# Performance work log

Measured on AMD Instinct MI355X. Metric: run time of the kernel, lower is better.

Reference implementation:

```python
import jax, jax.numpy as jnp
import numpy as np

B, S, E = 4, 4096, 1024
H = 16
D = E // H            # per-head dim (k_dim == v_dim == 64)
N_SAMPLE = 1024       # tokens kept per (batch, head)


def setup_inputs() -> dict:
    key = jax.random.key(0)
    ks = jax.random.split(key, 7)
    lim = float(np.sqrt(6.0 / (E + E)))  # xavier_uniform for square weight
    x = jax.random.normal(ks[0], (B, S, E), dtype=jnp.float32)
    Wq = jax.random.uniform(ks[1], (E, E), jnp.float32, -lim, lim)
    Wk = jax.random.uniform(ks[2], (E, E), jnp.float32, -lim, lim)
    Wv = jax.random.uniform(ks[3], (E, E), jnp.float32, -lim, lim)
    bq = jnp.zeros((E,), jnp.float32)
    bk = jnp.zeros((E,), jnp.float32)
    bv = jnp.zeros((E,), jnp.float32)
    return {"x": x, "Wq": Wq, "bq": bq, "Wk": Wk, "bk": bk, "Wv": Wv, "bv": bv}


def reference(x, Wq, bq, Wk, bk, Wv, bv):
    Bs, Sl, Ed = x.shape
    # projections -> [B, H, S, D]
    q = (x @ Wq.T + bq).reshape(Bs, Sl, H, D).transpose(0, 2, 1, 3)
    k = (x @ Wk.T + bk).reshape(Bs, Sl, H, D).transpose(0, 2, 1, 3)
    v = (x @ Wv.T + bv).reshape(Bs, Sl, H, D).transpose(0, 2, 1, 3)

    # cosFormer feature map: relu + cos/sin positional reweighting
    pos = jnp.arange(Sl, dtype=x.dtype)
    theta = (jnp.pi / 2.0) * pos / Sl            # [S]
    cos_w = jnp.cos(theta)[None, None, :, None]  # [1,1,S,1]
    sin_w = jnp.sin(theta)[None, None, :, None]
    qn = jax.nn.relu(q)
    kn = jax.nn.relu(k)
    q_cos, q_sin = qn * cos_w, qn * sin_w
    k_cos, k_sin = kn * cos_w, kn * sin_w

    # token sampler: top-N_SAMPLE tokens by (q*k).sum(-1) per (b,h)
    scores = jnp.sum(q * k, axis=-1)             # [B,H,S]
    _, idx = jax.lax.top_k(scores, N_SAMPLE)     # [B,H,n]

    # global K^T V reductions: [B,H,D,D]
    kv_cos = jnp.einsum("bhsd,bhse->bhde", k_cos, v)
    kv_sin = jnp.einsum("bhsd,bhse->bhde", k_sin, v)

    # gather sampled queries: [B,H,n,D]
    qs_cos = jnp.take_along_axis(q_cos, idx[..., None], axis=2)
    qs_sin = jnp.take_along_axis(q_sin, idx[..., None], axis=2)

    sampled = (jnp.einsum("bhnd,bhde->bhne", qs_cos, kv_cos)
               + jnp.einsum("bhnd,bhde->bhne", qs_sin, kv_sin))  # [B,H,n,D]

    # scatter-add back into zeros at sampled positions
    bi = jnp.arange(Bs)[:, None, None]
    hi = jnp.arange(H)[None, :, None]
    values = jnp.zeros((Bs, H, Sl, D), sampled.dtype).at[bi, hi, idx].add(sampled)

    out = values.transpose(0, 2, 1, 3).reshape(Bs, Sl, H * D)
    return out  # o_proj is Identity (v_dim*num_heads == embed_dim); dropout=0
```

## Files before the change

kernel.cpp:

```cpp
#include <hip/hip_runtime.h>
#include <hip/hip_bf16.h>

#define B_ 4
#define S_ 4096
#define E_ 1024
#define H_ 16
#define D_ 64
#define NS_ 1024
#define M_ (B_*S_)
#define K_ E_
#define DELTA 0.12f
#define BANDCAP 96

typedef __attribute__((ext_vector_type(8))) short bf16x8;
typedef __attribute__((ext_vector_type(4))) float floatx4;

#define THSTEP 0.00038349519697141023f

__device__ inline float bf16_to_f(unsigned short u) {
    return __uint_as_float(((unsigned)u) << 16);
}
__device__ inline unsigned short f_to_bf16(float f) {
    unsigned u = __float_as_uint(f);
    unsigned r = (u + 0x7FFFu + ((u >> 16) & 1u)) >> 16;
    return (unsigned short)r;
}

__device__ inline void gl_lds16(const void* g, void* l) {
    __builtin_amdgcn_global_load_lds(
        (const __attribute__((address_space(1))) void*)g,
        (__attribute__((address_space(3))) void*)l, 16, 0, 0);
}

__global__ __launch_bounds__(256) void split_x_kernel(
    const float* __restrict__ x, ushort* __restrict__ xh)
{
    int i = blockIdx.x * 256 + threadIdx.x;
    float4 v = ((const float4*)x)[i];
    ushort4 hh;
    hh.x = f_to_bf16(v.x); hh.y = f_to_bf16(v.y);
    hh.z = f_to_bf16(v.z); hh.w = f_to_bf16(v.w);
    ((ushort4*)xh)[i] = hh;
}

__global__ __launch_bounds__(256) void split_w_kernel(
    const float* __restrict__ Wq, const float* __restrict__ Wk,
    const float* __restrict__ Wv,
    ushort* __restrict__ Wqh, ushort* __restrict__ Wql,
    ushort* __restrict__ Wkh, ushort* __restrict__ Wkl,
    ushort* __restrict__ Wvh)
{
    int i = blockIdx.x * 256 + threadIdx.x;
    float4 q = ((const float4*)Wq)[i];
    float4 k = ((const float4*)Wk)[i];
    float4 v = ((const float4*)Wv)[i];
    ushort4 h, l;
    h.x=f_to_bf16(q.x); l.x=f_to_bf16(q.x-bf16_to_f(h.x));
    h.y=f_to_bf16(q.y); l.y=f_to_bf16(q.y-bf16_to_f(h.y));
    h.z=f_to_bf16(q.z); l.z=f_to_bf16(q.z-bf16_to_f(h.z));
    h.w=f_to_bf16(q.w); l.w=f_to_bf16(q.w-bf16_to_f(h.w));
    ((ushort4*)Wqh)[i]=h; ((ushort4*)Wql)[i]=l;
    h.x=f_to_bf16(k.x); l.x=f_to_bf16(k.x-bf16_to_f(h.x));
    h.y=f_to_bf16(k.y); l.y=f_to_bf16(k.y-bf16_to_f(h.y));
    h.z=f_to_bf16(k.z); l.z=f_to_bf16(k.z-bf16_to_f(h.z));
    h.w=f_to_bf16(k.w); l.w=f_to_bf16(k.w-bf16_to_f(h.w));
    ((ushort4*)Wkh)[i]=h; ((ushort4*)Wkl)[i]=l;
    h.x=f_to_bf16(v.x); h.y=f_to_bf16(v.y);
    h.z=f_to_bf16(v.z); h.w=f_to_bf16(v.w);
    ((ushort4*)Wvh)[i]=h;
}

__global__ __launch_bounds__(256) void qkv_gemm(
    const ushort* __restrict__ xh,
    const ushort* __restrict__ Wqh, const ushort* __restrict__ Wql,
    const ushort* __restrict__ Wkh, const ushort* __restrict__ Wkl,
    const ushort* __restrict__ Wvh,
    const float* __restrict__ bq, const float* __restrict__ bk,
    const float* __restrict__ bv,
    float* __restrict__ q32, float* __restrict__ k32, ushort* __restrict__ v16)
{
    __shared__ __align__(16) ushort As[128 * 64];
    __shared__ __align__(16) ushort Bsh[128 * 64];
    __shared__ __align__(16) ushort Bsl[128 * 64];

    const int w = blockIdx.z;
    const ushort* Bhp = (w == 0) ? Wqh : (w == 1) ? Wkh : Wvh;
    const ushort* Blp = (w == 0) ? Wql : Wkl;
    const float* bias = (w == 0) ? bq : (w == 1) ? bk : bv;
    const bool lo = (w < 2);

    const int m0 = blockIdx.x * 128;
    const int n0 = blockIdx.y * 128;
    const int t = threadIdx.x;
    const int wave = t >> 6, lane = t & 63;
    const int wm = (wave >> 1) * 64, wn = (wave & 1) * 64;
    const int m16 = lane & 15, quad = lane >> 4;

    floatx4 acc[4][4];
#pragma unroll
    for (int i = 0; i < 4; i++)
#pragma unroll
        for (int j = 0; j < 4; j++) acc[i][j] = (floatx4){0.f, 0.f, 0.f, 0.f};

    int aoff[4], boff[4], lbase[4];
#pragma unroll
    for (int i = 0; i < 4; i++) {
        int slot = i * 256 + t;
        int r = slot >> 3, c = slot & 7, g = c ^ (r & 7);
        aoff[i] = (m0 + r) * K_ + g * 8;
        boff[i] = (n0 + r) * K_ + g * 8;
        lbase[i] = (i * 256 + wave * 64) * 8;
    }

    for (int ks = 0; ks < 16; ++ks) {
        const int kcol = ks * 64;
#pragma unroll
        for (int i = 0; i < 4; i++) {
            gl_lds16(xh + aoff[i] + kcol, &As[lbase[i]]);
            gl_lds16(Bhp + boff[i] + kcol, &Bsh[lbase[i]]);
        }
        if (lo) {
#pragma unroll
            for (int i = 0; i < 4; i++)
                gl_lds16(Blp + boff[i] + kcol, &Bsl[lbase[i]]);
        }
        __syncthreads();

#pragma unroll
        for (int kk = 0; kk < 2; ++kk) {
            bf16x8 af[4], bfr[4];
            const int g = kk * 4 + quad;
#pragma unroll
            for (int mt = 0; mt < 4; ++mt) {
                int r = wm + mt * 16 + m16;
                af[mt] = *(const bf16x8*)&As[(r * 8 + (g ^ (r & 7))) * 8];
            }
#pragma unroll
            for (int nt = 0; nt < 4; ++nt) {
                int r2 = wn + nt * 16 + m16;
                bfr[nt] = *(const bf16x8*)&Bsh[(r2 * 8 + (g ^ (r2 & 7))) * 8];
            }
#pragma unroll
            for (int mt = 0; mt < 4; ++mt)
#pragma unroll
                for (int nt = 0; nt < 4; ++nt)
                    acc[mt][nt] = __builtin_amdgcn_mfma_f32_16x16x32_bf16(
                        af[mt], bfr[nt], acc[mt][nt], 0, 0, 0);
            if (lo) {
#pragma unroll
                for (int nt = 0; nt < 4; ++nt) {
                    int r2 = wn + nt * 16 + m16;
                    bfr[nt] = *(const bf16x8*)&Bsl[(r2 * 8 + (g ^ (r2 & 7))) * 8];
                }
#pragma unroll
                for (int mt = 0; mt < 4; ++mt)
#pragma unroll
                    for (int nt = 0; nt < 4; ++nt)
                        acc[mt][nt] = __builtin_amdgcn_mfma_f32_16x16x32_bf16(
                            af[mt], bfr[nt], acc[mt][nt], 0, 0, 0);
            }
        }
        __syncthreads();
    }

    float biasv[4];
#pragma unroll
    for (int nt = 0; nt < 4; nt++)
        biasv[nt] = bias[n0 + wn + nt * 16 + m16];

    if (w < 2) {
        float* dst = (w == 0) ? q32 : k32;
#pragma unroll
        for (int mt = 0; mt < 4; ++mt)
#pragma unroll
            for (int nt = 0; nt < 4; ++nt) {
                int colg = n0 + wn + nt * 16 + m16;
#pragma unroll
                for (int reg = 0; reg < 4; ++reg) {
                    int rowg = m0 + wm + mt * 16 + quad * 4 + reg;
                    dst[(size_t)rowg * E_ + colg] = acc[mt][nt][reg] + biasv[nt];
                }
            }
    } else {
#pragma unroll
        for (int mt = 0; mt < 4; ++mt)
#pragma unroll
            for (int nt = 0; nt < 4; ++nt) {
                int colg = n0 + wn + nt * 16 + m16;
#pragma unroll
                for (int reg = 0; reg < 4; ++reg) {
                    int rowg = m0 + wm + mt * 16 + quad * 4 + reg;
                    v16[(size_t)rowg * E_ + colg] = f_to_bf16(acc[mt][nt][reg] + biasv[nt]);
                }
            }
    }
}

__global__ __launch_bounds__(256) void scores_kernel(
    const float* __restrict__ q32, const float* __restrict__ k32,
    float* __restrict__ scores)
{
    int wid = blockIdx.x * 4 + (threadIdx.x >> 6);
    int lane = threadIdx.x & 63;
    int s = wid & (S_ - 1);
    int bh = wid >> 12;
    int b = bh >> 4, h = bh & 15;
    size_t addr = (size_t)(b * S_ + s) * E_ + h * 64 + lane;
    float p = q32[addr] * k32[addr];
#pragma unroll
    for (int m = 32; m; m >>= 1) p += __shfl_xor(p, m, 64);
    if (lane == 0) scores[wid] = p;
}

__global__ __launch_bounds__(256) void band_select_kernel(
    const float* __restrict__ scores, int* __restrict__ selidx,
    int* __restrict__ band, int* __restrict__ meta)
{
    __shared__ unsigned keys[4096];
    __shared__ unsigned hist[256];
    __shared__ unsigned suf[256];
    __shared__ unsigned bcast[2];
    __shared__ int cnt_in, cnt_band;

    int bh = blockIdx.x;
    int t = threadIdx.x;
    const float* sc = scores + (size_t)bh * S_;

    for (int i = t; i < 4096; i += 256) {
        unsigned u = __float_as_uint(sc[i]);
        u = (u & 0x80000000u) ? ~u : (u | 0x80000000u);
        keys[i] = u;
    }
    if (t == 0) { cnt_in = 0; cnt_band = 0; }
    __syncthreads();

    unsigned prefix = 0, want = NS_;
    for (int shift = 24; shift >= 0; shift -= 8) {
        hist[t] = 0;
        __syncthreads();
        unsigned pmask = (shift == 24) ? 0u : (0xFFFFFFFFu << (shift + 8));
        for (int i = t; i < 4096; i += 256) {
            unsigned ky = keys[i];
            if ((ky & pmask) == prefix) atomicAdd(&hist[(ky >> shift) & 255u], 1u);
        }
        __syncthreads();
        suf[t] = hist[t];
        __syncthreads();
        for (int off = 1; off < 256; off <<= 1) {
            unsigned add = (t + off < 256) ? suf[t + off] : 0u;
            __syncthreads();
            suf[t] += add;
            __syncthreads();
        }
        unsigned Sb = suf[t];
        unsigned Snx = (t < 255) ? suf[t + 1] : 0u;
        if (Sb >= want && Snx < want) {
            bcast[0] = (unsigned)t;
            bcast[1] = want - Snx;
        }
        __syncthreads();
        prefix = prefix | (bcast[0] << shift);
        want = bcast[1];
        __syncthreads();
    }
    unsigned fb = (prefix & 0x80000000u) ? (prefix ^ 0x80000000u) : ~prefix;
    float Ta = __uint_as_float(fb);
    float Thi = Ta + DELTA, Tlo = Ta - DELTA;

    int* sel = selidx + (size_t)bh * NS_;
    int* bnd = band + (size_t)bh * BANDCAP;
    for (int i = t; i < 4096; i += 256) {
        float v = sc[i];
        if (v > Thi) {
            int p = atomicAdd(&cnt_in, 1);
            sel[p] = i;
        } else if (v >= Tlo) {
            int p = atomicAdd(&cnt_band, 1);
            if (p < BANDCAP) bnd[p] = i;
        }
    }
    __syncthreads();
    if (t == 0) {
        meta[bh * 2 + 0] = cnt_in;
        meta[bh * 2 + 1] = (cnt_band < BANDCAP) ? cnt_band : BANDCAP;
    }
}

__global__ __launch_bounds__(512) void band_exact_kernel(
    const float* __restrict__ x,
    const float* __restrict__ Wq, const float* __restrict__ Wk,
    const int* __restrict__ band, const int* __restrict__ meta,
    double* __restrict__ bscore)
{
    int j = blockIdx.x, bh = blockIdx.y;
    int NB = meta[bh * 2 + 1];
    if (j >= NB) return;
    int b = bh >> 4, h = bh & 15;
    int s = band[(size_t)bh * BANDCAP + j];
    int t = threadIdx.x;
    int wave = t >> 6, lane = t & 63;

    __shared__ float xs[1024];
    __shared__ double qkd[128];

    if (t < 256)
        *(float4*)&xs[t * 4] = *(const float4*)(x + (size_t)(b * S_ + s) * K_ + t * 4);
    __syncthreads();

    const float* Wbase = (wave < 4) ? Wq : Wk;
    int role = wave >> 2;
    int dbase = (wave & 3) * 16;
    const float4* xs4 = (const float4*)xs;

    for (int rr = 0; rr < 16; ++rr) {
        int d = dbase + rr;
        const float4* wrow4 = (const float4*)(Wbase + (size_t)(h * 64 + d) * K_);
        double a = 0.0;
#pragma unroll
        for (int p = 0; p < 4; ++p) {
            float4 wv = wrow4[lane + 64 * p];
            float4 xv = xs4[lane + 64 * p];
            a += (double)xv.x * wv.x + (double)xv.y * wv.y
               + (double)xv.z * wv.z + (double)xv.w * wv.w;
        }
#pragma unroll
        for (int m = 32; m; m >>= 1) a += __shfl_xor(a, m, 64);
        if (lane == 0) qkd[role * 64 + d] = a;
    }
    __syncthreads();

    if (t < 64) {
        double p = qkd[t] * qkd[64 + t];
#pragma unroll
        for (int m = 32; m; m >>= 1) p += __shfl_xor(p, m, 64);
        if (t == 0) bscore[(size_t)bh * BANDCAP + j] = p;
    }
}

__global__ __launch_bounds__(128) void band_rank_kernel(
    const double* __restrict__ bscore, const int* __restrict__ band,
    const int* __restrict__ meta, int* __restrict__ selidx)
{
    __shared__ double sc[BANDCAP];
    __shared__ int bi[BANDCAP];
    int bh = blockIdx.x, t = threadIdx.x;
    int cnt_in = meta[bh * 2 + 0], NB = meta[bh * 2 + 1];
    int need = NS_ - cnt_in;
    if (t < NB) {
        sc[t] = bscore[(size_t)bh * BANDCAP + t];
        bi[t] = band[(size_t)bh * BANDCAP + t];
    }
    __syncthreads();
    if (t < NB) {
        double mine = sc[t]; int myi = bi[t]; int r = 0;
        for (int j2 = 0; j2 < NB; ++j2)
            r += (sc[j2] > mine) || (sc[j2] == mine && bi[j2] < myi);
        if (r < need) selidx[(size_t)bh * NS_ + cnt_in + r] = myi;
    }
}

__global__ __launch_bounds__(256) void kv_partial_kernel(
    const float* __restrict__ k32, const ushort* __restrict__ v16,
    float* __restrict__ kvp)
{
    __shared__ float kls[16 * 64];
    __shared__ float vls[16 * 64];
    int ch = blockIdx.x;
    int bh = blockIdx.y;
    int b = bh >> 4, h = bh & 15;
    int t = threadIdx.x;
    int d0 = (t >> 4) * 4, e0 = (t & 15) * 4;
    int lr = t >> 4, lc = (t & 15) * 4;

    float accC[4][4] = {}, accS[4][4] = {};
    const float* kbase = k32 + (size_t)b * S_ * E_ + h * 64;
    const ushort* vbase = v16 + (size_t)b * S_ * E_ + h * 64;
    int s0 = ch * 256;

    for (int g = 0; g < 16; ++g) {
        int srow = s0 + g * 16 + lr;
        float4 kf = *(const float4*)(kbase + (size_t)srow * E_ + lc);
        ushort4 vu = *(const ushort4*)(vbase + (size_t)srow * E_ + lc);
        __syncthreads();
        *(float4*)&kls[lr * 64 + lc] = kf;
        float4 vf = { bf16_to_f(vu.x), bf16_to_f(vu.y),
                      bf16_to_f(vu.z), bf16_to_f(vu.w) };
        *(float4*)&vls[lr * 64 + lc] = vf;
        __syncthreads();
#pragma unroll 4
        for (int si = 0; si < 16; ++si) {
            int s = s0 + g * 16 + si;
            float th = (float)s * THSTEP;
            float cw = __cosf(th), sw = __sinf(th);
            float4 kf2 = *(const float4*)&kls[si * 64 + d0];
            float4 vf2 = *(const float4*)&vls[si * 64 + e0];
            float kr[4] = { fmaxf(kf2.x, 0.f), fmaxf(kf2.y, 0.f),
                            fmaxf(kf2.z, 0.f), fmaxf(kf2.w, 0.f) };
            float vv[4] = { vf2.x, vf2.y, vf2.z, vf2.w };
            float kc[4], ksn[4];
#pragma unroll
            for (int i = 0; i < 4; i++) { kc[i] = kr[i] * cw; ksn[i] = kr[i] * sw; }
#pragma unroll
            for (int i = 0; i < 4; i++)
#pragma unroll
                for (int jj = 0; jj < 4; jj++) {
                    accC[i][jj] += kc[i] * vv[jj];
                    accS[i][jj] += ksn[i] * vv[jj];
                }
        }
    }
    float* pc = kvp + ((size_t)(bh * 16 + ch) * 2) * 4096;
    float* ps = pc + 4096;
#pragma unroll
    for (int i = 0; i < 4; i++)
#pragma unroll
        for (int jj = 0; jj < 4; jj++) {
            pc[(d0 + i) * 64 + (e0 + jj)] = accC[i][jj];
            ps[(d0 + i) * 64 + (e0 + jj)] = accS[i][jj];
        }
}

__global__ __launch_bounds__(256) void kv_reduce_kernel(
    const float* __restrict__ kvp, float* __restrict__ kv)
{
    int i = blockIdx.x * 256 + threadIdx.x;
    if (i >= 64 * 2 * 4096) return;
    int bh = i >> 13;
    int rem = i & 8191;
    const float* p = kvp + (size_t)bh * 16 * 8192 + rem;
    float a = 0.f;
#pragma unroll
    for (int c = 0; c < 16; c++) a += p[c * 8192];
    kv[i] = a;
}

__global__ __launch_bounds__(256) void sampled_kernel(
    const float* __restrict__ q32, const int* __restrict__ selidx,
    const float* __restrict__ kv, float* __restrict__ out)
{
    __shared__ float kvc[4096];
    __shared__ float kvs[4096];
    __shared__ float qs[256 * 65];
    __shared__ int sidx[256];
    int bh = blockIdx.y;
    int b = bh >> 4, h = bh & 15;
    int t = threadIdx.x;
    int wave = t >> 6, lane = t & 63;

    const float* kvsrc = kv + (size_t)bh * 8192;
    for (int i = t; i < 4096; i += 256) {
        kvc[i] = kvsrc[i];
        kvs[i] = kvsrc[4096 + i];
    }
    sidx[t] = selidx[(size_t)bh * NS_ + blockIdx.x * 256 + t];
    __syncthreads();

    for (int i = 0; i < 64; ++i) {
        int row = wave * 64 + i;
        int sr = sidx[row];
        qs[row * 65 + lane] = q32[(size_t)(b * S_ + sr) * E_ + h * 64 + lane];
    }
    __syncthreads();

    int s = sidx[t];
    float th = (float)s * THSTEP;
    float cw = __cosf(th), sw = __sinf(th);

    float acc[64];
#pragma unroll
    for (int e = 0; e < 64; e++) acc[e] = 0.f;

    for (int d = 0; d < 64; ++d) {
        float qd = fmaxf(qs[t * 65 + d], 0.f);
        float a = qd * cw, bb = qd * sw;
        const float4* pc4 = (const float4*)&kvc[d * 64];
        const float4* ps4 = (const float4*)&kvs[d * 64];
#pragma unroll
        for (int e4 = 0; e4 < 16; e4++) {
            float4 c4 = pc4[e4], s4 = ps4[e4];
            acc[e4 * 4 + 0] += a * c4.x + bb * s4.x;
            acc[e4 * 4 + 1] += a * c4.y + bb * s4.y;
            acc[e4 * 4 + 2] += a * c4.z + bb * s4.z;
            acc[e4 * 4 + 3] += a * c4.w + bb * s4.w;
        }
    }
    __syncthreads();
#pragma unroll
    for (int e = 0; e < 64; e++) qs[t * 65 + e] = acc[e];
    __syncthreads();

    for (int i = 0; i < 64; ++i) {
        int row = wave * 64 + i;
        int sr = sidx[row];
        out[(size_t)(b * S_ + sr) * E_ + h * 64 + lane] = qs[row * 65 + lane];
    }
}

__global__ void zero_kernel(uint4* __restrict__ p, int n16)
{
    int stride = gridDim.x * blockDim.x;
    for (int i = blockIdx.x * blockDim.x + threadIdx.x; i < n16; i += stride)
        p[i] = make_uint4(0u, 0u, 0u, 0u);
}

extern "C" void kernel_launch(void* const* d_in, const int* in_sizes, int n_in,
                              void* d_out, int out_size, void* d_ws, size_t ws_size,
                              hipStream_t stream)
{
    const float* x  = (const float*)d_in[0];
    const float* Wq = (const float*)d_in[1];
    const float* bq = (const float*)d_in[2];
    const float* Wk = (const float*)d_in[3];
    const float* bk = (const float*)d_in[4];
    const float* Wv = (const float*)d_in[5];
    const float* bv = (const float*)d_in[6];

    char* ws = (char*)d_ws;
    ushort* xh     = (ushort*)(ws);
    float*  kvp    = (float*)(ws);
    float*  q32    = (float*)(ws + 33554432);
    float*  k32    = (float*)(ws + 100663296);
    ushort* v16    = (ushort*)(ws + 167772160);
    ushort* Wqh    = (ushort*)(ws + 201326592);
    ushort* Wql    = (ushort*)(ws + 203423744);
    ushort* Wkh    = (ushort*)(ws + 205520896);
    ushort* Wkl    = (ushort*)(ws + 207618048);
    ushort* Wvh    = (ushort*)(ws + 209715200);
    float*  scores = (float*)(ws + 211812352);
    int*    selidx = (int*)(ws + 212860928);
    int*    band   = (int*)(ws + 213123072);
    double* bscore = (double*)(ws + 213147648);
    int*    meta   = (int*)(ws + 213196800);
    float*  kv     = (float*)(ws + 213197312);
    float*  out    = (float*)d_out;

    hipLaunchKernelGGL(zero_kernel, dim3(2048), dim3(256), 0, stream,
                       (uint4*)out, (int)((size_t)M_ * E_ * 4 / 16));
    hipLaunchKernelGGL(split_x_kernel, dim3((M_ * K_) / 1024), dim3(256), 0, stream,
                       x, xh);
    hipLaunchKernelGGL(split_w_kernel, dim3((E_ * E_) / 1024), dim3(256), 0, stream,
                       Wq, Wk, Wv, Wqh, Wql, Wkh, Wkl, Wvh);
    hipLaunchKernelGGL(qkv_gemm, dim3(128, 8, 3), dim3(256), 0, stream,
                       xh, Wqh, Wql, Wkh, Wkl, Wvh, bq, bk, bv, q32, k32, v16);
    hipLaunchKernelGGL(scores_kernel, dim3((B_ * H_ * S_) / 4), dim3(256), 0, stream,
                       q32, k32, scores);
    hipLaunchKernelGGL(band_select_kernel, dim3(B_ * H_), dim3(256), 0, stream,
                       scores, selidx, band, meta);
    hipLaunchKernelGGL(band_exact_kernel, dim3(BANDCAP, B_ * H_), dim3(512), 0, stream,
                       x, Wq, Wk, band, meta, bscore);
    hipLaunchKernelGGL(band_rank_kernel, dim3(B_ * H_), dim3(128), 0, stream,
                       bscore, band, meta, selidx);
    hipLaunchKernelGGL(kv_partial_kernel, dim3(16, 64), dim3(256), 0, stream,
                       k32, v16, kvp);
    hipLaunchKernelGGL(kv_reduce_kernel, dim3(2048), dim3(256), 0, stream,
                       kvp, kv);
    hipLaunchKernelGGL(sampled_kernel, dim3(NS_ / 256, B_ * H_), dim3(256), 0, stream,
                       q32, selidx, kv, out);
}
```

Baseline: 550.0 us.

## Compute KV partial reductions with bf16 MFMA using hi/lo split of K features

Result: faster. 509.8 us (-7.3%).

```diff
diff --git a/kernel.cpp b/kernel.cpp
--- a/kernel.cpp
+++ b/kernel.cpp
@@ -359,65 +359,123 @@
     }
 }
 
-__global__ __launch_bounds__(256) void kv_partial_kernel(
+__global__ __launch_bounds__(256) void kv_mfma_kernel(
     const float* __restrict__ k32, const ushort* __restrict__ v16,
     float* __restrict__ kvp)
 {
-    __shared__ float kls[16 * 64];
-    __shared__ float vls[16 * 64];
-    int ch = blockIdx.x;
-    int bh = blockIdx.y;
-    int b = bh >> 4, h = bh & 15;
-    int t = threadIdx.x;
-    int d0 = (t >> 4) * 4, e0 = (t & 15) * 4;
-    int lr = t >> 4, lc = (t & 15) * 4;
-
-    float accC[4][4] = {}, accS[4][4] = {};
-    const float* kbase = k32 + (size_t)b * S_ * E_ + h * 64;
-    const ushort* vbase = v16 + (size_t)b * S_ * E_ + h * 64;
-    int s0 = ch * 256;
-
-    for (int g = 0; g < 16; ++g) {
-        int srow = s0 + g * 16 + lr;
-        float4 kf = *(const float4*)(kbase + (size_t)srow * E_ + lc);
-        ushort4 vu = *(const ushort4*)(vbase + (size_t)srow * E_ + lc);
-        __syncthreads();
-        *(float4*)&kls[lr * 64 + lc] = kf;
-        float4 vf = { bf16_to_f(vu.x), bf16_to_f(vu.y),
-                      bf16_to_f(vu.z), bf16_to_f(vu.w) };
-        *(float4*)&vls[lr * 64 + lc] = vf;
-        __syncthreads();
-#pragma unroll 4
-        for (int si = 0; si < 16; ++si) {
-            int s = s0 + g * 16 + si;
-            float th = (float)s * THSTEP;
-            float cw = __cosf(th), sw = __sinf(th);
-            float4 kf2 = *(const float4*)&kls[si * 64 + d0];
-            float4 vf2 = *(const float4*)&vls[si * 64 + e0];
-            float kr[4] = { fmaxf(kf2.x, 0.f), fmaxf(kf2.y, 0.f),
-                            fmaxf(kf2.z, 0.f), fmaxf(kf2.w, 0.f) };
-            float vv[4] = { vf2.x, vf2.y, vf2.z, vf2.w };
-            float kc[4], ksn[4];
-#pragma unroll
-            for (int i = 0; i < 4; i++) { kc[i] = kr[i] * cw; ksn[i] = kr[i] * sw; }
-#pragma unroll
-            for (int i = 0; i < 4; i++)
-#pragma unroll
-                for (int jj = 0; jj < 4; jj++) {
-                    accC[i][jj] += kc[i] * vv[jj];
-                    accS[i][jj] += ksn[i] * vv[jj];
+    __shared__ __align__(16) ushort P[5 * 64 * 88];
+
+    const int ch = blockIdx.x;
+    const int bh = blockIdx.y;
+    const int b = bh >> 4, h = bh & 15;
+    const int t = threadIdx.x;
+    const int wave = t >> 6, lane = t & 63;
+    const int m16 = lane & 15, quad = lane >> 4;
+    const int wm = (wave >> 1) * 32, wn = (wave & 1) * 32;
+    const int d0 = wave * 16;
+
+    const float*  kbase = k32 + (size_t)b * S_ * E_ + h * 64 + d0;
+    const ushort* vbase = v16 + (size_t)b * S_ * E_ + h * 64 + d0;
+
+    floatx4 acc[2][2][2];
+#pragma unroll
+    for (int p = 0; p < 2; p++)
+#pragma unroll
+        for (int i = 0; i < 2; i++)
+#pragma unroll
+            for (int j = 0; j < 2; j++) acc[p][i][j] = (floatx4){0.f,0.f,0.f,0.f};
+
+    float  ka[16];
+    ushort va[16];
+    int sg = ch * 256 + lane;
+    {
+        const float*  kr = kbase + (size_t)sg * E_;
+        const ushort* vr = vbase + (size_t)sg * E_;
+#pragma unroll
+        for (int j = 0; j < 4; ++j) *(float4*)&ka[j * 4] = ((const float4*)kr)[j];
+        *(uint4*)&va[0] = *(const uint4*)vr;
+        *(uint4*)&va[8] = *(const uint4*)(vr + 8);
+    }
+
+    for (int grp = 0; grp < 4; ++grp) {
+        float th = (float)sg * THSTEP;
+        float cw = __cosf(th), sw = __sinf(th);
+        int s_loc = lane;
+
+        __syncthreads();
+#pragma unroll
+        for (int j = 0; j < 16; ++j) {
+            float kr_ = fmaxf(ka[j], 0.f);
+            float pc = kr_ * cw, ps = kr_ * sw;
+            ushort chh = f_to_bf16(pc);
+            ushort cll = f_to_bf16(pc - bf16_to_f(chh));
+            ushort shh = f_to_bf16(ps);
+            ushort sll = f_to_bf16(ps - bf16_to_f(shh));
+            int r = (d0 + j) * 88 + s_loc;
+            P[0 * 5632 + r] = chh;
+            P[1 * 5632 + r] = cll;
+            P[2 * 5632 + r] = shh;
+            P[3 * 5632 + r] = sll;
+            P[4 * 5632 + r] = va[j];
+        }
+        __syncthreads();
+
+        if (grp < 3) {
+            sg += 64;
+            const float*  kr = kbase + (size_t)sg * E_;
+            const ushort* vr = vbase + (size_t)sg * E_;
+#pragma unroll
+            for (int j = 0; j < 4; ++j) *(float4*)&ka[j * 4] = ((const float4*)kr)[j];
+            *(uint4*)&va[0] = *(const uint4*)vr;
+            *(uint4*)&va[8] = *(const uint4*)(vr + 8);
+        }
+
+#pragma unroll
+        for (int kk = 0; kk < 2; ++kk) {
+            const int so = kk * 32 + quad * 8;
+            bf16x8 ach[2], acl[2], ash[2], asl[2], bv[2];
+#pragma unroll
+            for (int mt = 0; mt < 2; ++mt) {
+                int r = (wm + mt * 16 + m16) * 88 + so;
+                ach[mt] = *(const bf16x8*)&P[0 * 5632 + r];
+                acl[mt] = *(const bf16x8*)&P[1 * 5632 + r];
+                ash[mt] = *(const bf16x8*)&P[2 * 5632 + r];
+                asl[mt] = *(const bf16x8*)&P[3 * 5632 + r];
+            }
+#pragma unroll
+            for (int nt = 0; nt < 2; ++nt) {
+                int r = (wn + nt * 16 + m16) * 88 + so;
+                bv[nt] = *(const bf16x8*)&P[4 * 5632 + r];
+            }
+#pragma unroll
+            for (int mt = 0; mt < 2; ++mt)
+#pragma unroll
+                for (int nt = 0; nt < 2; ++nt) {
+                    acc[0][mt][nt] = __builtin_amdgcn_mfma_f32_16x16x32_bf16(
+                        ach[mt], bv[nt], acc[0][mt][nt], 0, 0, 0);
+                    acc[0][mt][nt] = __builtin_amdgcn_mfma_f32_16x16x32_bf16(
+                        acl[mt], bv[nt], acc[0][mt][nt], 0, 0, 0);
+                    acc[1][mt][nt] = __builtin_amdgcn_mfma_f32_16x16x32_bf16(
+                        ash[mt], bv[nt], acc[1][mt][nt], 0, 0, 0);
+                    acc[1][mt][nt] = __builtin_amdgcn_mfma_f32_16x16x32_bf16(
+                        asl[mt], bv[nt], acc[1][mt][nt], 0, 0, 0);
                 }
         }
     }
-    float* pc = kvp + ((size_t)(bh * 16 + ch) * 2) * 4096;
-    float* ps = pc + 4096;
-#pragma unroll
-    for (int i = 0; i < 4; i++)
-#pragma unroll
-        for (int jj = 0; jj < 4; jj++) {
-            pc[(d0 + i) * 64 + (e0 + jj)] = accC[i][jj];
-            ps[(d0 + i) * 64 + (e0 + jj)] = accS[i][jj];
-        }
+
+    float* base = kvp + ((size_t)(bh * 16 + ch) * 2) * 4096;
+#pragma unroll
+    for (int p = 0; p < 2; ++p)
+#pragma unroll
+        for (int mt = 0; mt < 2; ++mt)
+#pragma unroll
+            for (int nt = 0; nt < 2; ++nt)
+#pragma unroll
+                for (int reg = 0; reg < 4; ++reg) {
+                    int row = wm + mt * 16 + quad * 4 + reg;
+                    int col = wn + nt * 16 + m16;
+                    base[p * 4096 + row * 64 + col] = acc[p][mt][nt][reg];
+                }
 }
 
 __global__ __launch_bounds__(256) void kv_reduce_kernel(
@@ -550,7 +608,7 @@
                        x, Wq, Wk, band, meta, bscore);
     hipLaunchKernelGGL(band_rank_kernel, dim3(B_ * H_), dim3(128), 0, stream,
                        bscore, band, meta, selidx);
-    hipLaunchKernelGGL(kv_partial_kernel, dim3(16, 64), dim3(256), 0, stream,
+    hipLaunchKernelGGL(kv_mfma_kernel, dim3(16, 64), dim3(256), 0, stream,
                        k32, v16, kvp);
     hipLaunchKernelGGL(kv_reduce_kernel, dim3(2048), dim3(256), 0, stream,
                        kvp, kv);
```
